# Performance work log

Measured on AMD Instinct MI355X. Metric: run time of the kernel, lower is better.

## Reference

```python
import jax, jax.numpy as jnp
import numpy as np

B, N, DIM = 4, 2048, 64  # batch, seq_len (== gate out dim), model dim (== dim_head)
H, DH = 8, 64            # heads, dim_head


def setup_inputs() -> dict:
    key = jax.random.key(0)
    ks = jax.random.split(key, 12)
    inner = H * DH
    inp = {
        'q': jax.random.normal(ks[0], (B, N, DIM), jnp.float32),
        'k': jax.random.normal(ks[1], (B, N, DIM), jnp.float32),
        'v': jax.random.normal(ks[2], (B, N, DIM), jnp.float32),
        'Wq': jax.random.normal(ks[3], (inner, DIM), jnp.float32) * 0.05,
        'Wk': jax.random.normal(ks[4], (inner, DIM), jnp.float32) * 0.05,
        'Wv': jax.random.normal(ks[5], (inner, DIM), jnp.float32) * 0.05,
        'Wo': jax.random.normal(ks[6], (DIM, inner), jnp.float32) * 0.05,
        'bo': jax.random.normal(ks[7], (DIM,), jnp.float32) * 0.05,
        'Wg': jax.random.normal(ks[8], (N, DIM), jnp.float32) * 0.05,
        's_local': jnp.float32(1.0),
        's_long': jnp.float32(1.0),
        # recurrent compressive-memory state; positive to avoid 0/0 of zero-init buffers
        'mem': jax.random.uniform(ks[9], (H, DH, DH), jnp.float32) + 0.5,
        'mem_norm': jax.random.uniform(ks[10], (H, N, 1), jnp.float32) + 0.5,
    }
    return inp


def _heads(x, W):
    # x: (B,N,DIM) @ W.T (DIM, H*DH) -> (B,H,N,DH)
    y = x @ W.T
    return y.reshape(x.shape[0], x.shape[1], H, DH).transpose(0, 2, 1, 3)


def reference(q, k, v, Wq, Wk, Wv, Wo, bo, Wg, s_local, s_long, mem, mem_norm):
    scale = DH ** -0.5
    qh, kh, vh = _heads(q, Wq), _heads(k, Wk), _heads(v, Wv)  # (B,H,N,DH)

    # local softmax attention, down-gated by (1 - sigmoid(local scalar))
    sim = jnp.einsum('bhnd,bhmd->bhnm', qh, kh) * scale
    local_attn = jax.nn.softmax(sim, axis=-1) * (1.0 - jax.nn.sigmoid(s_local))

    # query compressive memory: elu(q) @ M / (elu(q) * norm)
    eq = jax.nn.elu(qh)
    mem_q = jnp.einsum('bhnd,hde->bhne', eq, mem) / (eq * mem_norm[None])  # (B,H,N,DH)
    gated = jax.nn.sigmoid(s_long) * jnp.einsum('bhnd,md->bhnm', mem_q, Wg)  # (B,H,N,N)

    attn = local_attn + gated
    out = jnp.einsum('bhnm,bhmd->bhnd', attn, vh)
    out = out.transpose(0, 2, 1, 3).reshape(q.shape[0], q.shape[1], H * DH)
    out = out @ Wo.T + bo  # (B,N,DIM)

    # memory update (state side effect in the original forward)
    ek = jax.nn.elu(kh)
    v_term = vh - jnp.einsum('bhnd,hde->bhne', ek, mem) / (ek * mem_norm[None])
    new_mem = mem[None] + jnp.einsum('bhnd,bhne->bhde', ek, v_term)  # (B,H,DH,DH)
    new_norm = ek.sum(-1)  # (B,H,N)
    return out, new_mem, new_norm
```

## Files before the change

### kernel.cpp

```cpp
#include <hip/hip_runtime.h>
#include <math.h>


#define B_   4
#define N_   2048
#define H_   8
#define BH_  32
#define KP   72

typedef __bf16 bf16x8 __attribute__((ext_vector_type(8)));
typedef __bf16 bf16x4 __attribute__((ext_vector_type(4)));
typedef float  f32x4  __attribute__((ext_vector_type(4)));

__device__ __forceinline__ float eluf(float x) {
    return x > 0.0f ? x : expm1f(x);
}

__global__ __launch_bounds__(256) void k_proj(
    const float* __restrict__ q, const float* __restrict__ k, const float* __restrict__ v,
    const float* __restrict__ Wq, const float* __restrict__ Wk, const float* __restrict__ Wv,
    __bf16* __restrict__ qb, float* __restrict__ kh, __bf16* __restrict__ kb,
    __bf16* __restrict__ vb, __bf16* __restrict__ vbT)
{
    const int which = blockIdx.z;
    const float* __restrict__ src = (which == 0) ? q : (which == 1) ? k : v;
    const float* __restrict__ W   = (which == 0) ? Wq : (which == 1) ? Wk : Wv;
    const int h    = blockIdx.y;
    const int row0 = blockIdx.x * 64;

    __shared__ __align__(16) float AsT[64][68];
    __shared__ __align__(16) float WsT[64][68];
    const int tid = threadIdx.x;
    for (int s = 0; s < 16; ++s) {
        int flat = s * 256 + tid;
        int r = flat >> 6, d = flat & 63;
        AsT[d][r] = src[(size_t)(row0 + r) * 64 + d];
        WsT[d][r] = W[(size_t)(h * 64 + r) * 64 + d];
    }
    __syncthreads();

    const int ty = tid >> 4, tx = tid & 15;
    float acc[4][4];
    #pragma unroll
    for (int i = 0; i < 4; ++i)
        #pragma unroll
        for (int j = 0; j < 4; ++j) acc[i][j] = 0.0f;
    for (int kd = 0; kd < 64; ++kd) {
        float4 a4 = *(const float4*)&AsT[kd][ty * 4];
        float4 w4 = *(const float4*)&WsT[kd][tx * 4];
        float a[4] = {a4.x, a4.y, a4.z, a4.w};
        float w[4] = {w4.x, w4.y, w4.z, w4.w};
        #pragma unroll
        for (int i = 0; i < 4; ++i)
            #pragma unroll
            for (int j = 0; j < 4; ++j) acc[i][j] = fmaf(a[i], w[j], acc[i][j]);
    }

    const int b = row0 >> 11, nb = row0 & 2047;
    if (which == 0) {
        #pragma unroll
        for (int i = 0; i < 4; ++i) {
            size_t idx = ((((size_t)b * H_ + h) * N_ + nb + ty * 4 + i) << 6) + tx * 4;
            bf16x4 o4 = {(__bf16)acc[i][0], (__bf16)acc[i][1],
                         (__bf16)acc[i][2], (__bf16)acc[i][3]};
            *(bf16x4*)&qb[idx] = o4;
        }
    } else if (which == 1) {
        #pragma unroll
        for (int i = 0; i < 4; ++i) {
            size_t idx = ((((size_t)b * H_ + h) * N_ + nb + ty * 4 + i) << 6) + tx * 4;
            *(float4*)&kh[idx] = make_float4(acc[i][0], acc[i][1], acc[i][2], acc[i][3]);
            bf16x4 o4 = {(__bf16)acc[i][0], (__bf16)acc[i][1],
                         (__bf16)acc[i][2], (__bf16)acc[i][3]};
            *(bf16x4*)&kb[idx] = o4;
        }
    } else {
        #pragma unroll
        for (int i = 0; i < 4; ++i) {
            size_t idx = ((((size_t)b * H_ + h) * N_ + nb + ty * 4 + i) << 6) + tx * 4;
            bf16x4 o4 = {(__bf16)acc[i][0], (__bf16)acc[i][1],
                         (__bf16)acc[i][2], (__bf16)acc[i][3]};
            *(bf16x4*)&vb[idx] = o4;
        }
        __syncthreads();
        #pragma unroll
        for (int i = 0; i < 4; ++i)
            #pragma unroll
            for (int j = 0; j < 4; ++j) WsT[tx * 4 + j][ty * 4 + i] = acc[i][j];
        __syncthreads();
        const int e = tid >> 2, nc = (tid & 3) * 16;
        bf16x8 lo, hi;
        #pragma unroll
        for (int jj = 0; jj < 8; ++jj) {
            lo[jj] = (__bf16)WsT[e][nc + jj];
            hi[jj] = (__bf16)WsT[e][nc + 8 + jj];
        }
        size_t base = (((size_t)b * H_ + h) * 64 + e) * (size_t)N_ + nb + nc;
        *(bf16x8*)&vbT[base]     = lo;
        *(bf16x8*)&vbT[base + 8] = hi;
    }
}

__global__ __launch_bounds__(256) void k_memacc(
    const float* __restrict__ kh, const __bf16* __restrict__ vb,
    const float* __restrict__ mem, const float* __restrict__ mem_norm,
    float* __restrict__ pmem, float* __restrict__ out_norm)
{
    const int chunk = blockIdx.x;
    const int bh    = blockIdx.y;
    const int h     = bh & 7;
    const int n0    = chunk * 128;

    __shared__ __align__(16) __bf16 memT_hi[64 * KP], memT_lo[64 * KP];
    __shared__ __align__(16) __bf16 ekn_hi[64 * KP],  ekn_lo[64 * KP];
    __shared__ __align__(16) __bf16 ekT_hi[64 * KP],  ekT_lo[64 * KP];
    __shared__ __align__(16) __bf16 vtT_hi[64 * KP],  vtT_lo[64 * KP];

    const int tid  = threadIdx.x;
    const int w    = tid >> 6, lane = tid & 63;
    const int quad = lane >> 4, m = lane & 15;

    for (int s = 0; s < 16; ++s) {
        int flat = s * 256 + tid;
        int d = flat >> 6, e = flat & 63;
        float mv = mem[(size_t)h * 4096 + flat];
        __bf16 hi = (__bf16)mv;
        memT_hi[e * KP + d] = hi;
        memT_lo[e * KP + d] = (__bf16)(mv - (float)hi);
    }

    f32x4 accM[4];
    #pragma unroll
    for (int t = 0; t < 4; ++t) { f32x4 z = {0.f, 0.f, 0.f, 0.f}; accM[t] = z; }
    __syncthreads();

    for (int sub = 0; sub < 2; ++sub) {
        const int nb = n0 + sub * 64;
        for (int rr = w; rr < 64; rr += 4) {
            const int n = nb + rr;
            float ekv = eluf(kh[((size_t)bh * N_ + n) * 64 + lane]);
            __bf16 hi = (__bf16)ekv;
            __bf16 lo = (__bf16)(ekv - (float)hi);
            ekn_hi[rr * KP + lane] = hi;
            ekn_lo[rr * KP + lane] = lo;
            ekT_hi[lane * KP + rr] = hi;
            ekT_lo[lane * KP + rr] = lo;
            float srt = ekv;
            #pragma unroll
            for (int m2 = 32; m2; m2 >>= 1) srt += __shfl_xor(srt, m2, 64);
            if (lane == 0) out_norm[(size_t)bh * N_ + n] = srt;
        }
        __syncthreads();

        f32x4 km[4];
        #pragma unroll
        for (int t = 0; t < 4; ++t) { f32x4 z = {0.f, 0.f, 0.f, 0.f}; km[t] = z; }
        #pragma unroll
        for (int c2 = 0; c2 < 2; ++c2) {
            bf16x8 Ah = *(const bf16x8*)&ekn_hi[(w * 16 + m) * KP + c2 * 32 + quad * 8];
            bf16x8 Al = *(const bf16x8*)&ekn_lo[(w * 16 + m) * KP + c2 * 32 + quad * 8];
            #pragma unroll
            for (int et = 0; et < 4; ++et) {
                bf16x8 Bh = *(const bf16x8*)&memT_hi[(et * 16 + m) * KP + c2 * 32 + quad * 8];
                bf16x8 Bl = *(const bf16x8*)&memT_lo[(et * 16 + m) * KP + c2 * 32 + quad * 8];
                km[et] = __builtin_amdgcn_mfma_f32_16x16x32_bf16(Al, Bh, km[et], 0, 0, 0);
                km[et] = __builtin_amdgcn_mfma_f32_16x16x32_bf16(Ah, Bl, km[et], 0, 0, 0);
                km[et] = __builtin_amdgcn_mfma_f32_16x16x32_bf16(Ah, Bh, km[et], 0, 0, 0);
            }
        }
        float nrmv[4];
        #pragma unroll
        for (int r = 0; r < 4; ++r)
            nrmv[r] = mem_norm[(size_t)h * N_ + nb + w * 16 + quad * 4 + r];
        #pragma unroll
        for (int et = 0; et < 4; ++et) {
            #pragma unroll
            for (int r = 0; r < 4; ++r) {
                const int nl = w * 16 + quad * 4 + r;
                const int e  = et * 16 + m;
                float vh  = (float)vb[((size_t)bh * N_ + nb + nl) * 64 + e];
                float ekv = (float)ekn_hi[nl * KP + e] + (float)ekn_lo[nl * KP + e];
                float vt  = vh - km[et][r] / (ekv * nrmv[r]);
                __bf16 hi = (__bf16)vt;
                vtT_hi[e * KP + nl] = hi;
                vtT_lo[e * KP + nl] = (__bf16)(vt - (float)hi);
            }
        }
        __syncthreads();

        #pragma unroll
        for (int c2 = 0; c2 < 2; ++c2) {
            bf16x8 Ah = *(const bf16x8*)&ekT_hi[(w * 16 + m) * KP + c2 * 32 + quad * 8];
            bf16x8 Al = *(const bf16x8*)&ekT_lo[(w * 16 + m) * KP + c2 * 32 + quad * 8];
            #pragma unroll
            for (int et = 0; et < 4; ++et) {
                bf16x8 Bh = *(const bf16x8*)&vtT_hi[(et * 16 + m) * KP + c2 * 32 + quad * 8];
                bf16x8 Bl = *(const bf16x8*)&vtT_lo[(et * 16 + m) * KP + c2 * 32 + quad * 8];
                accM[et] = __builtin_amdgcn_mfma_f32_16x16x32_bf16(Al, Bh, accM[et], 0, 0, 0);
                accM[et] = __builtin_amdgcn_mfma_f32_16x16x32_bf16(Ah, Bl, accM[et], 0, 0, 0);
                accM[et] = __builtin_amdgcn_mfma_f32_16x16x32_bf16(Ah, Bh, accM[et], 0, 0, 0);
            }
        }
        __syncthreads();
    }

    const size_t base = ((size_t)chunk * BH_ + bh) * 4096;
    #pragma unroll
    for (int et = 0; et < 4; ++et)
        #pragma unroll
        for (int r = 0; r < 4; ++r)
            pmem[base + (size_t)(w * 16 + quad * 4 + r) * 64 + et * 16 + m] =
                accM[et][r];
}

__global__ __launch_bounds__(256) void k_gv(
    const float* __restrict__ Wg, const __bf16* __restrict__ vbT,
    float* __restrict__ pGv)
{
    const int chunk = blockIdx.x;
    const int bh    = blockIdx.y;
    const int n0    = chunk * 128;
    __shared__ __align__(16) __bf16 WgT[64 * 136];
    const int tid  = threadIdx.x;
    const int w    = tid >> 6, lane = tid & 63;
    const int quad = lane >> 4, m = tid & 15;

    for (int s = 0; s < 8; ++s) {
        int f4 = s * 256 + tid;
        int n = f4 >> 4, dg = (f4 & 15) * 4;
        float4 wv = *(const float4*)&Wg[(size_t)(n0 + n) * 64 + dg];
        WgT[(dg + 0) * 136 + n] = (__bf16)wv.x;
        WgT[(dg + 1) * 136 + n] = (__bf16)wv.y;
        WgT[(dg + 2) * 136 + n] = (__bf16)wv.z;
        WgT[(dg + 3) * 136 + n] = (__bf16)wv.w;
    }
    __syncthreads();

    f32x4 acc[4];
    #pragma unroll
    for (int t = 0; t < 4; ++t) { f32x4 z = {0.f, 0.f, 0.f, 0.f}; acc[t] = z; }
    #pragma unroll
    for (int c = 0; c < 4; ++c) {
        bf16x8 Af = *(const bf16x8*)&WgT[(w * 16 + m) * 136 + c * 32 + quad * 8];
        #pragma unroll
        for (int et = 0; et < 4; ++et) {
            bf16x8 Bf = *(const bf16x8*)&vbT[((size_t)bh * 64 + et * 16 + m) * N_ +
                                             n0 + c * 32 + quad * 8];
            acc[et] = __builtin_amdgcn_mfma_f32_16x16x32_bf16(Af, Bf, acc[et], 0, 0, 0);
        }
    }
    const size_t base = ((size_t)chunk * BH_ + bh) * 4096;
    #pragma unroll
    for (int et = 0; et < 4; ++et)
        #pragma unroll
        for (int r = 0; r < 4; ++r)
            pGv[base + (size_t)(w * 16 + quad * 4 + r) * 64 + et * 16 + m] =
                acc[et][r];
}

__global__ __launch_bounds__(256) void k_reduce(
    const float* __restrict__ mem, const float* __restrict__ pmem,
    const float* __restrict__ pGv, float* __restrict__ out_mem, float* __restrict__ Gv)
{
    const int idx = blockIdx.x * 256 + threadIdx.x;
    const int bh = idx >> 12, h = bh & 7, de = idx & 4095;
    float sm = mem[(size_t)h * 4096 + de];
    float sg = 0.0f;
    #pragma unroll
    for (int c = 0; c < 16; ++c) {
        sm += pmem[(size_t)c * 131072 + idx];
        sg += pGv[(size_t)c * 131072 + idx];
    }
    out_mem[idx] = sm;
    Gv[idx] = sg;
}

__global__ __launch_bounds__(256, 4) void k_flash(
    const __bf16* __restrict__ qb, const __bf16* __restrict__ kb,
    const __bf16* __restrict__ vbT, const float* __restrict__ mem,
    const float* __restrict__ mem_norm, const float* __restrict__ Gv,
    const float* __restrict__ s_local_p, const float* __restrict__ s_long_p,
    __bf16* __restrict__ o)
{
    const int n0 = blockIdx.x * 128;
    const int bh = blockIdx.y;
    const int h  = bh & 7;
    const __bf16* __restrict__ kbp = kb  + (size_t)bh * N_ * 64;
    const __bf16* __restrict__ vtp = vbT + (size_t)bh * 64 * N_;

    __shared__ __align__(16) __bf16 Kb[64 * KP];
    __shared__ __align__(16) __bf16 VT[64 * KP];
    __shared__ __align__(16) __bf16 Pw[128 * KP];
    __shared__ float lsl[128];
    __shared__ float nrm_l[128];

    const int tid  = threadIdx.x;
    const int w    = tid >> 6, lane = tid & 63;
    const int quad = lane >> 4, m = lane & 15;
    const float gl   = 1.0f - 1.0f / (1.0f + __expf(-s_local_p[0]));
    const float sigg = 1.0f / (1.0f + __expf(-s_long_p[0]));

    if (tid < 128) nrm_l[tid] = mem_norm[(size_t)h * N_ + n0 + tid];

    const size_t q0 = ((size_t)bh * N_ + n0 + w * 32 + m) * 64;
    const size_t q1 = q0 + 16 * 64;
    bf16x8 qa00 = *(const bf16x8*)&qb[q0 + quad * 8];
    bf16x8 qa01 = *(const bf16x8*)&qb[q0 + 32 + quad * 8];
    bf16x8 qa10 = *(const bf16x8*)&qb[q1 + quad * 8];
    bf16x8 qa11 = *(const bf16x8*)&qb[q1 + 32 + quad * 8];

    f32x4 O0[4], O1[4];
    #pragma unroll
    for (int t = 0; t < 4; ++t) {
        f32x4 z = {0.f, 0.f, 0.f, 0.f};
        O0[t] = z; O1[t] = z;
    }
    float lsum0 = 0.f, lsum1 = 0.f;
    const int pr0 = w * 32, pr1 = w * 32 + 16;

    const int srow = tid >> 2, scg = (tid & 3) * 16;
    bf16x8 pk0 = *(const bf16x8*)&kbp[(size_t)srow * 64 + scg];
    bf16x8 pk1 = *(const bf16x8*)&kbp[(size_t)srow * 64 + scg + 8];
    bf16x8 pv0 = *(const bf16x8*)&vtp[(size_t)srow * N_ + scg];
    bf16x8 pv1 = *(const bf16x8*)&vtp[(size_t)srow * N_ + scg + 8];

    for (int c = 0; c < 32; ++c) {
        __syncthreads();
        *(bf16x8*)&Kb[srow * KP + scg]     = pk0;
        *(bf16x8*)&Kb[srow * KP + scg + 8] = pk1;
        *(bf16x8*)&VT[srow * KP + scg]     = pv0;
        *(bf16x8*)&VT[srow * KP + scg + 8] = pv1;
        __syncthreads();
        if (c + 1 < 32) {
            const size_t kn = (size_t)((c + 1) * 64 + srow) * 64 + scg;
            const size_t vn = (size_t)srow * N_ + (c + 1) * 64 + scg;
            pk0 = *(const bf16x8*)&kbp[kn];
            pk1 = *(const bf16x8*)&kbp[kn + 8];
            pv0 = *(const bf16x8*)&vtp[vn];
            pv1 = *(const bf16x8*)&vtp[vn + 8];
        }

        f32x4 s0[4], s1[4];
        #pragma unroll
        for (int t = 0; t < 4; ++t) {
            bf16x8 ka0 = *(const bf16x8*)&Kb[(t * 16 + m) * KP + quad * 8];
            bf16x8 ka1 = *(const bf16x8*)&Kb[(t * 16 + m) * KP + 32 + quad * 8];
            f32x4 z = {0.f, 0.f, 0.f, 0.f};
            z = __builtin_amdgcn_mfma_f32_16x16x32_bf16(ka0, qa00, z, 0, 0, 0);
            s0[t] = __builtin_amdgcn_mfma_f32_16x16x32_bf16(ka1, qa01, z, 0, 0, 0);
            f32x4 z2 = {0.f, 0.f, 0.f, 0.f};
            z2 = __builtin_amdgcn_mfma_f32_16x16x32_bf16(ka0, qa10, z2, 0, 0, 0);
            s1[t] = __builtin_amdgcn_mfma_f32_16x16x32_bf16(ka1, qa11, z2, 0, 0, 0);
        }

        #pragma unroll
        for (int t = 0; t < 4; ++t) {
            float p0 = __expf(s0[t][0] * 0.125f), p1 = __expf(s0[t][1] * 0.125f);
            float p2 = __expf(s0[t][2] * 0.125f), p3 = __expf(s0[t][3] * 0.125f);
            lsum0 += p0 + p1 + p2 + p3;
            bf16x4 pk = {(__bf16)p0, (__bf16)p1, (__bf16)p2, (__bf16)p3};
            *(bf16x4*)&Pw[(pr0 + m) * KP + t * 16 + quad * 4] = pk;
            float r0 = __expf(s1[t][0] * 0.125f), r1 = __expf(s1[t][1] * 0.125f);
            float r2 = __expf(s1[t][2] * 0.125f), r3 = __expf(s1[t][3] * 0.125f);
            lsum1 += r0 + r1 + r2 + r3;
            bf16x4 rk = {(__bf16)r0, (__bf16)r1, (__bf16)r2, (__bf16)r3};
            *(bf16x4*)&Pw[(pr1 + m) * KP + t * 16 + quad * 4] = rk;
        }
        asm volatile("s_waitcnt lgkmcnt(0)" ::: "memory");

        #pragma unroll
        for (int c2 = 0; c2 < 2; ++c2) {
            bf16x8 pa0 = *(const bf16x8*)&Pw[(pr0 + m) * KP + c2 * 32 + quad * 8];
            bf16x8 pa1 = *(const bf16x8*)&Pw[(pr1 + m) * KP + c2 * 32 + quad * 8];
            #pragma unroll
            for (int t = 0; t < 4; ++t) {
                bf16x8 vv = *(const bf16x8*)&VT[(t * 16 + m) * KP + c2 * 32 + quad * 8];
                O0[t] = __builtin_amdgcn_mfma_f32_16x16x32_bf16(pa0, vv, O0[t], 0, 0, 0);
                O1[t] = __builtin_amdgcn_mfma_f32_16x16x32_bf16(pa1, vv, O1[t], 0, 0, 0);
            }
        }
    }

    lsum0 += __shfl_xor(lsum0, 16, 64); lsum0 += __shfl_xor(lsum0, 32, 64);
    lsum1 += __shfl_xor(lsum1, 16, 64); lsum1 += __shfl_xor(lsum1, 32, 64);
    if (lane < 16) { lsl[pr0 + lane] = lsum0; lsl[pr1 + lane] = lsum1; }

    __syncthreads();
    for (int s2 = 0; s2 < 16; ++s2) {
        int flat = s2 * 256 + tid;
        int d = flat >> 6, e = flat & 63;
        Kb[e * KP + d] = (__bf16)mem[(size_t)h * 4096 + flat];
        VT[e * KP + d] = (__bf16)Gv[(size_t)bh * 4096 + flat];
    }
    __syncthreads();

    __bf16* op = o + ((size_t)bh * N_ + n0) * 64;
    #pragma unroll
    for (int s = 0; s < 2; ++s) {
        const int prs = w * 32 + s * 16;
        bf16x8 ea0, ea1;
        #pragma unroll
        for (int j = 0; j < 8; ++j) {
            ea0[j] = (__bf16)eluf((float)(s == 0 ? qa00[j] : qa10[j]));
            ea1[j] = (__bf16)eluf((float)(s == 0 ? qa01[j] : qa11[j]));
        }
        f32x4 num[4];
        #pragma unroll
        for (int t = 0; t < 4; ++t) {
            bf16x8 b0 = *(const bf16x8*)&Kb[(t * 16 + m) * KP + quad * 8];
            bf16x8 b1 = *(const bf16x8*)&Kb[(t * 16 + m) * KP + 32 + quad * 8];
            f32x4 z = {0.f, 0.f, 0.f, 0.f};
            z = __builtin_amdgcn_mfma_f32_16x16x32_bf16(ea0, b0, z, 0, 0, 0);
            num[t] = __builtin_amdgcn_mfma_f32_16x16x32_bf16(ea1, b1, z, 0, 0, 0);
        }
        *(bf16x8*)&Pw[(prs + m) * KP + quad * 8]      = ea0;
        *(bf16x8*)&Pw[(prs + m) * KP + 32 + quad * 8] = ea1;
        asm volatile("s_waitcnt lgkmcnt(0)" ::: "memory");
        float mq[4][4];
        #pragma unroll
        for (int t = 0; t < 4; ++t)
            #pragma unroll
            for (int r = 0; r < 4; ++r) {
                float eqv = (float)Pw[(prs + quad * 4 + r) * KP + t * 16 + m];
                mq[t][r] = num[t][r] / (eqv * nrm_l[prs + quad * 4 + r]);
            }
        #pragma unroll
        for (int t = 0; t < 4; ++t)
            #pragma unroll
            for (int r = 0; r < 4; ++r)
                Pw[(prs + quad * 4 + r) * KP + t * 16 + m] = (__bf16)mq[t][r];
        asm volatile("s_waitcnt lgkmcnt(0)" ::: "memory");
        bf16x8 ma0 = *(const bf16x8*)&Pw[(prs + m) * KP + quad * 8];
        bf16x8 ma1 = *(const bf16x8*)&Pw[(prs + m) * KP + 32 + quad * 8];

        #pragma unroll
        for (int t = 0; t < 4; ++t) {
            bf16x8 g0 = *(const bf16x8*)&VT[(t * 16 + m) * KP + quad * 8];
            bf16x8 g1 = *(const bf16x8*)&VT[(t * 16 + m) * KP + 32 + quad * 8];
            f32x4 z = {0.f, 0.f, 0.f, 0.f};
            z = __builtin_amdgcn_mfma_f32_16x16x32_bf16(ma0, g0, z, 0, 0, 0);
            f32x4 o2 = __builtin_amdgcn_mfma_f32_16x16x32_bf16(ma1, g1, z, 0, 0, 0);
            const f32x4 Oc = (s == 0) ? O0[t] : O1[t];
            #pragma unroll
            for (int r = 0; r < 4; ++r) {
                const int qr = prs + quad * 4 + r;
                float val = Oc[r] * (gl / lsl[qr]) + sigg * o2[r];
                op[(size_t)qr * 64 + t * 16 + m] = (__bf16)val;
            }
        }
    }
}

__global__ __launch_bounds__(256) void k_outproj(
    const __bf16* __restrict__ o, const float* __restrict__ Wo,
    const float* __restrict__ bo, float* __restrict__ out)
{
    const int row0 = blockIdx.x * 64;
    const int b = row0 >> 11, nb = row0 & 2047;
    __shared__ __align__(16) __bf16 WoS[64 * 40];
    const int tid  = threadIdx.x;
    const int w    = tid >> 6, lane = tid & 63;
    const int quad = lane >> 4, m = lane & 15;

    f32x4 acc[4];
    #pragma unroll
    for (int t = 0; t < 4; ++t) { f32x4 z = {0.f, 0.f, 0.f, 0.f}; acc[t] = z; }

    for (int kbk = 0; kbk < 16; ++kbk) {
        for (int s2 = 0; s2 < 8; ++s2) {
            int flat = s2 * 256 + tid;
            int n = flat >> 5, kk = flat & 31;
            WoS[n * 40 + kk] = (__bf16)Wo[(size_t)n * 512 + kbk * 32 + kk];
        }
        __syncthreads();
        const int hc = kbk >> 1;
        size_t arow = (((size_t)b * H_ + hc) * N_ + nb + w * 16 + m);
        bf16x8 af = *(const bf16x8*)&o[arow * 64 + (kbk & 1) * 32 + quad * 8];
        #pragma unroll
        for (int t = 0; t < 4; ++t) {
            bf16x8 bf_ = *(const bf16x8*)&WoS[(t * 16 + m) * 40 + quad * 8];
            acc[t] = __builtin_amdgcn_mfma_f32_16x16x32_bf16(af, bf_, acc[t], 0, 0, 0);
        }
        __syncthreads();
    }
    #pragma unroll
    for (int t = 0; t < 4; ++t) {
        float bias = bo[t * 16 + m];
        #pragma unroll
        for (int r = 0; r < 4; ++r)
            out[(size_t)(row0 + w * 16 + quad * 4 + r) * 64 + t * 16 + m] =
                acc[t][r] + bias;
    }
}

extern "C" void kernel_launch(void* const* d_in, const int* in_sizes, int n_in,
                              void* d_out, int out_size, void* d_ws, size_t ws_size,
                              hipStream_t stream)
{
    const float* q        = (const float*)d_in[0];
    const float* k        = (const float*)d_in[1];
    const float* v        = (const float*)d_in[2];
    const float* Wq       = (const float*)d_in[3];
    const float* Wk       = (const float*)d_in[4];
    const float* Wv       = (const float*)d_in[5];
    const float* Wo       = (const float*)d_in[6];
    const float* bo       = (const float*)d_in[7];
    const float* Wg       = (const float*)d_in[8];
    const float* s_local  = (const float*)d_in[9];
    const float* s_long   = (const float*)d_in[10];
    const float* mem      = (const float*)d_in[11];
    const float* mem_norm = (const float*)d_in[12];

    float* ws = (float*)d_ws;
    float*  kh  = ws;
    __bf16* qb  = (__bf16*)(ws + 4194304);
    __bf16* kb  = (__bf16*)(ws + 6291456);
    __bf16* vb  = (__bf16*)(ws + 8388608);
    __bf16* vbT = (__bf16*)(ws + 10485760);
    float*  Gv  = ws + 12582912;
    float*  pm  = ws + 12713984;
    float*  pg  = ws + 14811136;
    __bf16* o   = (__bf16*)(ws + 12713984);

    float* out      = (float*)d_out;
    float* out_mem  = out + 524288;
    float* out_norm = out + 655360;

    k_proj   <<<dim3(128, 8, 3), 256, 0, stream>>>(q, k, v, Wq, Wk, Wv,
                                                   qb, kh, kb, vb, vbT);
    k_memacc <<<dim3(16, 32),    256, 0, stream>>>(kh, vb, mem, mem_norm,
                                                   pm, out_norm);
    k_gv     <<<dim3(16, 32),    256, 0, stream>>>(Wg, vbT, pg);
    k_reduce <<<dim3(512),       256, 0, stream>>>(mem, pm, pg, out_mem, Gv);
    k_flash  <<<dim3(16, 32),    256, 0, stream>>>(qb, kb, vbT, mem, mem_norm, Gv,
                                                   s_local, s_long, o);
    k_outproj<<<dim3(128),       256, 0, stream>>>(o, Wo, bo, out);
}
```

Measured before the change: 221.7 us.

## Double-buffer K/V tiles via global_load_lds with XOR-swizzled layout

```diff
diff --git a/kernel.cpp b/kernel.cpp
--- a/kernel.cpp
+++ b/kernel.cpp
@@ -14,6 +14,12 @@
 
 __device__ __forceinline__ float eluf(float x) {
     return x > 0.0f ? x : expm1f(x);
+}
+
+__device__ __forceinline__ void gl2lds16(const void* g, void* l) {
+    __builtin_amdgcn_global_load_lds(
+        (const __attribute__((address_space(1))) unsigned int*)g,
+        (__attribute__((address_space(3))) unsigned int*)l, 16, 0, 0);
 }
 
 __global__ __launch_bounds__(256) void k_proj(
@@ -68,11 +74,13 @@
     } else if (which == 1) {
         #pragma unroll
         for (int i = 0; i < 4; ++i) {
-            size_t idx = ((((size_t)b * H_ + h) * N_ + nb + ty * 4 + i) << 6) + tx * 4;
-            *(float4*)&kh[idx] = make_float4(acc[i][0], acc[i][1], acc[i][2], acc[i][3]);
+            size_t rowbase = (((size_t)b * H_ + h) * N_ + nb + ty * 4 + i) << 6;
+            *(float4*)&kh[rowbase + tx * 4] =
+                make_float4(acc[i][0], acc[i][1], acc[i][2], acc[i][3]);
             bf16x4 o4 = {(__bf16)acc[i][0], (__bf16)acc[i][1],
                          (__bf16)acc[i][2], (__bf16)acc[i][3]};
-            *(bf16x4*)&kb[idx] = o4;
+            const int s = (ty * 4 + i) & 7;
+            *(bf16x4*)&kb[rowbase + (((tx >> 1) ^ s) << 3) + (tx & 1) * 4] = o4;
         }
     } else {
         #pragma unroll
@@ -95,9 +103,11 @@
             lo[jj] = (__bf16)WsT[e][nc + jj];
             hi[jj] = (__bf16)WsT[e][nc + 8 + jj];
         }
-        size_t base = (((size_t)b * H_ + h) * 64 + e) * (size_t)N_ + nb + nc;
-        *(bf16x8*)&vbT[base]     = lo;
-        *(bf16x8*)&vbT[base + 8] = hi;
+        size_t rowb = (((size_t)b * H_ + h) * 64 + e) * (size_t)N_ + nb;
+        const int j0 = (nc >> 3) ^ (e & 7);
+        const int j1 = ((nc >> 3) + 1) ^ (e & 7);
+        *(bf16x8*)&vbT[rowb + j0 * 8] = lo;
+        *(bf16x8*)&vbT[rowb + j1 * 8] = hi;
     }
 }
 
@@ -244,8 +254,9 @@
         bf16x8 Af = *(const bf16x8*)&WgT[(w * 16 + m) * 136 + c * 32 + quad * 8];
         #pragma unroll
         for (int et = 0; et < 4; ++et) {
+            const int jb = ((4 * c + quad) & 7) ^ (m & 7);
             bf16x8 Bf = *(const bf16x8*)&vbT[((size_t)bh * 64 + et * 16 + m) * N_ +
-                                             n0 + c * 32 + quad * 8];
+                                             n0 + (c >> 1) * 64 + jb * 8];
             acc[et] = __builtin_amdgcn_mfma_f32_16x16x32_bf16(Af, Bf, acc[et], 0, 0, 0);
         }
     }
@@ -288,8 +299,8 @@
     const __bf16* __restrict__ kbp = kb  + (size_t)bh * N_ * 64;
     const __bf16* __restrict__ vtp = vbT + (size_t)bh * 64 * N_;
 
-    __shared__ __align__(16) __bf16 Kb[64 * KP];
-    __shared__ __align__(16) __bf16 VT[64 * KP];
+    __shared__ __align__(16) __bf16 Kt[2][64 * 64];
+    __shared__ __align__(16) __bf16 Vt[2][64 * 64];
     __shared__ __align__(16) __bf16 Pw[128 * KP];
     __shared__ float lsl[128];
     __shared__ float nrm_l[128];
@@ -297,8 +308,10 @@
     const int tid  = threadIdx.x;
     const int w    = tid >> 6, lane = tid & 63;
     const int quad = lane >> 4, m = lane & 15;
+    const int sw   = m & 7;
     const float gl   = 1.0f - 1.0f / (1.0f + __expf(-s_local_p[0]));
     const float sigg = 1.0f / (1.0f + __expf(-s_long_p[0]));
+    const float SCL  = 0.18033688f;
 
     if (tid < 128) nrm_l[tid] = mem_norm[(size_t)h * N_ + n0 + tid];
 
@@ -318,33 +331,38 @@
     float lsum0 = 0.f, lsum1 = 0.f;
     const int pr0 = w * 32, pr1 = w * 32 + 16;
 
-    const int srow = tid >> 2, scg = (tid & 3) * 16;
-    bf16x8 pk0 = *(const bf16x8*)&kbp[(size_t)srow * 64 + scg];
-    bf16x8 pk1 = *(const bf16x8*)&kbp[(size_t)srow * 64 + scg + 8];
-    bf16x8 pv0 = *(const bf16x8*)&vtp[(size_t)srow * N_ + scg];
-    bf16x8 pv1 = *(const bf16x8*)&vtp[(size_t)srow * N_ + scg + 8];
+    const int r0 = w * 16 + (lane >> 3);
+    auto stage = [&](int c, int buf) {
+        const __bf16* gk0 = kbp + ((size_t)c * 64 + r0) * 64 + (lane & 7) * 8;
+        const __bf16* gv0 = vtp + (size_t)r0 * N_ + c * 64 + (lane & 7) * 8;
+        char* lk = (char*)&Kt[buf][0] + w * 2048;
+        char* lv = (char*)&Vt[buf][0] + w * 2048;
+        gl2lds16(gk0,            lk);
+        gl2lds16(gk0 + 8 * 64,   lk + 1024);
+        gl2lds16(gv0,            lv);
+        gl2lds16(gv0 + 8 * N_,   lv + 1024);
+    };
+
+    stage(0, 0);
 
     for (int c = 0; c < 32; ++c) {
-        __syncthreads();
-        *(bf16x8*)&Kb[srow * KP + scg]     = pk0;
-        *(bf16x8*)&Kb[srow * KP + scg + 8] = pk1;
-        *(bf16x8*)&VT[srow * KP + scg]     = pv0;
-        *(bf16x8*)&VT[srow * KP + scg + 8] = pv1;
-        __syncthreads();
+        const int buf = c & 1;
+        asm volatile("s_barrier" ::: "memory");
         if (c + 1 < 32) {
-            const size_t kn = (size_t)((c + 1) * 64 + srow) * 64 + scg;
-            const size_t vn = (size_t)srow * N_ + (c + 1) * 64 + scg;
-            pk0 = *(const bf16x8*)&kbp[kn];
-            pk1 = *(const bf16x8*)&kbp[kn + 8];
-            pv0 = *(const bf16x8*)&vtp[vn];
-            pv1 = *(const bf16x8*)&vtp[vn + 8];
-        }
+            stage(c + 1, buf ^ 1);
+            asm volatile("s_waitcnt vmcnt(4)" ::: "memory");
+        } else {
+            asm volatile("s_waitcnt vmcnt(0)" ::: "memory");
+        }
+        asm volatile("s_barrier" ::: "memory");
+        const __bf16* Kc = &Kt[buf][0];
+        const __bf16* Vc = &Vt[buf][0];
 
         f32x4 s0[4], s1[4];
         #pragma unroll
         for (int t = 0; t < 4; ++t) {
-            bf16x8 ka0 = *(const bf16x8*)&Kb[(t * 16 + m) * KP + quad * 8];
-            bf16x8 ka1 = *(const bf16x8*)&Kb[(t * 16 + m) * KP + 32 + quad * 8];
+            bf16x8 ka0 = *(const bf16x8*)&Kc[(t * 16 + m) * 64 + ((quad ^ sw) << 3)];
+            bf16x8 ka1 = *(const bf16x8*)&Kc[(t * 16 + m) * 64 + (((4 + quad) ^ sw) << 3)];
             f32x4 z = {0.f, 0.f, 0.f, 0.f};
             z = __builtin_amdgcn_mfma_f32_16x16x32_bf16(ka0, qa00, z, 0, 0, 0);
             s0[t] = __builtin_amdgcn_mfma_f32_16x16x32_bf16(ka1, qa01, z, 0, 0, 0);
@@ -355,15 +373,15 @@
 
         #pragma unroll
         for (int t = 0; t < 4; ++t) {
-            float p0 = __expf(s0[t][0] * 0.125f), p1 = __expf(s0[t][1] * 0.125f);
-            float p2 = __expf(s0[t][2] * 0.125f), p3 = __expf(s0[t][3] * 0.125f);
+            float p0 = exp2f(s0[t][0] * SCL), p1 = exp2f(s0[t][1] * SCL);
+            float p2 = exp2f(s0[t][2] * SCL), p3 = exp2f(s0[t][3] * SCL);
             lsum0 += p0 + p1 + p2 + p3;
             bf16x4 pk = {(__bf16)p0, (__bf16)p1, (__bf16)p2, (__bf16)p3};
             *(bf16x4*)&Pw[(pr0 + m) * KP + t * 16 + quad * 4] = pk;
-            float r0 = __expf(s1[t][0] * 0.125f), r1 = __expf(s1[t][1] * 0.125f);
-            float r2 = __expf(s1[t][2] * 0.125f), r3 = __expf(s1[t][3] * 0.125f);
-            lsum1 += r0 + r1 + r2 + r3;
-            bf16x4 rk = {(__bf16)r0, (__bf16)r1, (__bf16)r2, (__bf16)r3};
+            float r0_ = exp2f(s1[t][0] * SCL), r1_ = exp2f(s1[t][1] * SCL);
+            float r2_ = exp2f(s1[t][2] * SCL), r3_ = exp2f(s1[t][3] * SCL);
+            lsum1 += r0_ + r1_ + r2_ + r3_;
+            bf16x4 rk = {(__bf16)r0_, (__bf16)r1_, (__bf16)r2_, (__bf16)r3_};
             *(bf16x4*)&Pw[(pr1 + m) * KP + t * 16 + quad * 4] = rk;
         }
         asm volatile("s_waitcnt lgkmcnt(0)" ::: "memory");
@@ -374,7 +392,8 @@
             bf16x8 pa1 = *(const bf16x8*)&Pw[(pr1 + m) * KP + c2 * 32 + quad * 8];
             #pragma unroll
             for (int t = 0; t < 4; ++t) {
-                bf16x8 vv = *(const bf16x8*)&VT[(t * 16 + m) * KP + c2 * 32 + quad * 8];
+                bf16x8 vv = *(const bf16x8*)&Vc[(t * 16 + m) * 64 +
+                                                (((c2 * 4 + quad) ^ sw) << 3)];
                 O0[t] = __builtin_amdgcn_mfma_f32_16x16x32_bf16(pa0, vv, O0[t], 0, 0, 0);
                 O1[t] = __builtin_amdgcn_mfma_f32_16x16x32_bf16(pa1, vv, O1[t], 0, 0, 0);
             }
@@ -386,11 +405,13 @@
     if (lane < 16) { lsl[pr0 + lane] = lsum0; lsl[pr1 + lane] = lsum1; }
 
     __syncthreads();
+    __bf16* MT = &Kt[0][0];
+    __bf16* GT = &Vt[0][0];
     for (int s2 = 0; s2 < 16; ++s2) {
         int flat = s2 * 256 + tid;
         int d = flat >> 6, e = flat & 63;
-        Kb[e * KP + d] = (__bf16)mem[(size_t)h * 4096 + flat];
-        VT[e * KP + d] = (__bf16)Gv[(size_t)bh * 4096 + flat];
+        MT[e * KP + d] = (__bf16)mem[(size_t)h * 4096 + flat];
+        GT[e * KP + d] = (__bf16)Gv[(size_t)bh * 4096 + flat];
     }
     __syncthreads();
 
@@ -407,8 +428,8 @@
         f32x4 num[4];
         #pragma unroll
         for (int t = 0; t < 4; ++t) {
-            bf16x8 b0 = *(const bf16x8*)&Kb[(t * 16 + m) * KP + quad * 8];
-            bf16x8 b1 = *(const bf16x8*)&Kb[(t * 16 + m) * KP + 32 + quad * 8];
+            bf16x8 b0 = *(const bf16x8*)&MT[(t * 16 + m) * KP + quad * 8];
+            bf16x8 b1 = *(const bf16x8*)&MT[(t * 16 + m) * KP + 32 + quad * 8];
             f32x4 z = {0.f, 0.f, 0.f, 0.f};
             z = __builtin_amdgcn_mfma_f32_16x16x32_bf16(ea0, b0, z, 0, 0, 0);
             num[t] = __builtin_amdgcn_mfma_f32_16x16x32_bf16(ea1, b1, z, 0, 0, 0);
@@ -435,16 +456,16 @@
 
         #pragma unroll
         for (int t = 0; t < 4; ++t) {
-            bf16x8 g0 = *(const bf16x8*)&VT[(t * 16 + m) * KP + quad * 8];
-            bf16x8 g1 = *(const bf16x8*)&VT[(t * 16 + m) * KP + 32 + quad * 8];
+            bf16x8 g0 = *(const bf16x8*)&GT[(t * 16 + m) * KP + quad * 8];
+            bf16x8 g1 = *(const bf16x8*)&GT[(t * 16 + m) * KP + 32 + quad * 8];
             f32x4 z = {0.f, 0.f, 0.f, 0.f};
             z = __builtin_amdgcn_mfma_f32_16x16x32_bf16(ma0, g0, z, 0, 0, 0);
             f32x4 o2 = __builtin_amdgcn_mfma_f32_16x16x32_bf16(ma1, g1, z, 0, 0, 0);
-            const f32x4 Oc = (s == 0) ? O0[t] : O1[t];
             #pragma unroll
             for (int r = 0; r < 4; ++r) {
                 const int qr = prs + quad * 4 + r;
-                float val = Oc[r] * (gl / lsl[qr]) + sigg * o2[r];
+                float val = ((s == 0) ? O0[t][r] : O1[t][r]) * (gl / lsl[qr])
+                            + sigg * o2[r];
                 op[(size_t)qr * 64 + t * 16 + m] = (__bf16)val;
             }
         }
```

After: 237.1 us. 6.9% more time.

## Split flash attention over key halves and add separate combine kernel

Applied to the files above, without the earlier changes.

```diff
diff --git a/kernel.cpp b/kernel.cpp
--- a/kernel.cpp
+++ b/kernel.cpp
@@ -277,30 +277,23 @@
 
 __global__ __launch_bounds__(256, 4) void k_flash(
     const __bf16* __restrict__ qb, const __bf16* __restrict__ kb,
-    const __bf16* __restrict__ vbT, const float* __restrict__ mem,
-    const float* __restrict__ mem_norm, const float* __restrict__ Gv,
-    const float* __restrict__ s_local_p, const float* __restrict__ s_long_p,
-    __bf16* __restrict__ o)
-{
-    const int n0 = blockIdx.x * 128;
-    const int bh = blockIdx.y;
-    const int h  = bh & 7;
+    const __bf16* __restrict__ vbT, __bf16* __restrict__ Opart,
+    float* __restrict__ lsp)
+{
+    const int n0   = blockIdx.x * 128;
+    const int half = blockIdx.y;
+    const int bh   = blockIdx.z;
     const __bf16* __restrict__ kbp = kb  + (size_t)bh * N_ * 64;
     const __bf16* __restrict__ vtp = vbT + (size_t)bh * 64 * N_;
 
     __shared__ __align__(16) __bf16 Kb[64 * KP];
     __shared__ __align__(16) __bf16 VT[64 * KP];
     __shared__ __align__(16) __bf16 Pw[128 * KP];
-    __shared__ float lsl[128];
-    __shared__ float nrm_l[128];
 
     const int tid  = threadIdx.x;
     const int w    = tid >> 6, lane = tid & 63;
     const int quad = lane >> 4, m = lane & 15;
-    const float gl   = 1.0f - 1.0f / (1.0f + __expf(-s_local_p[0]));
-    const float sigg = 1.0f / (1.0f + __expf(-s_long_p[0]));
-
-    if (tid < 128) nrm_l[tid] = mem_norm[(size_t)h * N_ + n0 + tid];
+    const float SCL = 0.18033688f;
 
     const size_t q0 = ((size_t)bh * N_ + n0 + w * 32 + m) * 64;
     const size_t q1 = q0 + 16 * 64;
@@ -319,19 +312,21 @@
     const int pr0 = w * 32, pr1 = w * 32 + 16;
 
     const int srow = tid >> 2, scg = (tid & 3) * 16;
-    bf16x8 pk0 = *(const bf16x8*)&kbp[(size_t)srow * 64 + scg];
-    bf16x8 pk1 = *(const bf16x8*)&kbp[(size_t)srow * 64 + scg + 8];
-    bf16x8 pv0 = *(const bf16x8*)&vtp[(size_t)srow * N_ + scg];
-    bf16x8 pv1 = *(const bf16x8*)&vtp[(size_t)srow * N_ + scg + 8];
-
-    for (int c = 0; c < 32; ++c) {
+    const int c0 = half * 16;
+    bf16x8 pk0 = *(const bf16x8*)&kbp[(size_t)(c0 * 64 + srow) * 64 + scg];
+    bf16x8 pk1 = *(const bf16x8*)&kbp[(size_t)(c0 * 64 + srow) * 64 + scg + 8];
+    bf16x8 pv0 = *(const bf16x8*)&vtp[(size_t)srow * N_ + c0 * 64 + scg];
+    bf16x8 pv1 = *(const bf16x8*)&vtp[(size_t)srow * N_ + c0 * 64 + scg + 8];
+
+    for (int cc = 0; cc < 16; ++cc) {
+        const int c = c0 + cc;
         __syncthreads();
         *(bf16x8*)&Kb[srow * KP + scg]     = pk0;
         *(bf16x8*)&Kb[srow * KP + scg + 8] = pk1;
         *(bf16x8*)&VT[srow * KP + scg]     = pv0;
         *(bf16x8*)&VT[srow * KP + scg + 8] = pv1;
         __syncthreads();
-        if (c + 1 < 32) {
+        if (cc + 1 < 16) {
             const size_t kn = (size_t)((c + 1) * 64 + srow) * 64 + scg;
             const size_t vn = (size_t)srow * N_ + (c + 1) * 64 + scg;
             pk0 = *(const bf16x8*)&kbp[kn];
@@ -355,13 +350,13 @@
 
         #pragma unroll
         for (int t = 0; t < 4; ++t) {
-            float p0 = __expf(s0[t][0] * 0.125f), p1 = __expf(s0[t][1] * 0.125f);
-            float p2 = __expf(s0[t][2] * 0.125f), p3 = __expf(s0[t][3] * 0.125f);
+            float p0 = exp2f(s0[t][0] * SCL), p1 = exp2f(s0[t][1] * SCL);
+            float p2 = exp2f(s0[t][2] * SCL), p3 = exp2f(s0[t][3] * SCL);
             lsum0 += p0 + p1 + p2 + p3;
             bf16x4 pk = {(__bf16)p0, (__bf16)p1, (__bf16)p2, (__bf16)p3};
             *(bf16x4*)&Pw[(pr0 + m) * KP + t * 16 + quad * 4] = pk;
-            float r0 = __expf(s1[t][0] * 0.125f), r1 = __expf(s1[t][1] * 0.125f);
-            float r2 = __expf(s1[t][2] * 0.125f), r3 = __expf(s1[t][3] * 0.125f);
+            float r0 = exp2f(s1[t][0] * SCL), r1 = exp2f(s1[t][1] * SCL);
+            float r2 = exp2f(s1[t][2] * SCL), r3 = exp2f(s1[t][3] * SCL);
             lsum1 += r0 + r1 + r2 + r3;
             bf16x4 rk = {(__bf16)r0, (__bf16)r1, (__bf16)r2, (__bf16)r3};
             *(bf16x4*)&Pw[(pr1 + m) * KP + t * 16 + quad * 4] = rk;
@@ -383,72 +378,133 @@
 
     lsum0 += __shfl_xor(lsum0, 16, 64); lsum0 += __shfl_xor(lsum0, 32, 64);
     lsum1 += __shfl_xor(lsum1, 16, 64); lsum1 += __shfl_xor(lsum1, 32, 64);
-    if (lane < 16) { lsl[pr0 + lane] = lsum0; lsl[pr1 + lane] = lsum1; }
-
-    __syncthreads();
+    const size_t lbase = ((size_t)half * BH_ + bh) * N_ + n0;
+    if (lane < 16) {
+        lsp[lbase + pr0 + lane] = lsum0;
+        lsp[lbase + pr1 + lane] = lsum1;
+    }
+
+    __bf16* op = Opart + (((size_t)half * BH_ + bh) * N_ + n0) * 64;
+    #pragma unroll
+    for (int t = 0; t < 4; ++t)
+        #pragma unroll
+        for (int r = 0; r < 4; ++r) {
+            op[(size_t)(pr0 + quad * 4 + r) * 64 + t * 16 + m] = (__bf16)O0[t][r];
+            op[(size_t)(pr1 + quad * 4 + r) * 64 + t * 16 + m] = (__bf16)O1[t][r];
+        }
+}
+
+__global__ __launch_bounds__(256, 4) void k_combine(
+    const __bf16* __restrict__ Opart, const float* __restrict__ lsp,
+    const __bf16* __restrict__ qb, const float* __restrict__ mem,
+    const float* __restrict__ mem_norm, const float* __restrict__ Gv,
+    const float* __restrict__ s_local_p, const float* __restrict__ s_long_p,
+    __bf16* __restrict__ o)
+{
+    const int n0 = blockIdx.x * 64;
+    const int bh = blockIdx.y;
+    const int h  = bh & 7;
+
+    __shared__ __align__(16) __bf16 MT[64 * KP];
+    __shared__ __align__(16) __bf16 GT[64 * KP];
+    __shared__ __align__(16) __bf16 Pc[64 * KP];
+    __shared__ float lsl[64];
+    __shared__ float nrm_l[64];
+
+    const int tid  = threadIdx.x;
+    const int w    = tid >> 6, lane = tid & 63;
+    const int quad = lane >> 4, m = lane & 15;
+    const float gl   = 1.0f - 1.0f / (1.0f + __expf(-s_local_p[0]));
+    const float sigg = 1.0f / (1.0f + __expf(-s_long_p[0]));
+
+    if (tid < 64) {
+        lsl[tid] = lsp[(size_t)bh * N_ + n0 + tid] +
+                   lsp[((size_t)BH_ + bh) * N_ + n0 + tid];
+        nrm_l[tid] = mem_norm[(size_t)h * N_ + n0 + tid];
+    }
     for (int s2 = 0; s2 < 16; ++s2) {
         int flat = s2 * 256 + tid;
         int d = flat >> 6, e = flat & 63;
-        Kb[e * KP + d] = (__bf16)mem[(size_t)h * 4096 + flat];
-        VT[e * KP + d] = (__bf16)Gv[(size_t)bh * 4096 + flat];
+        MT[e * KP + d] = (__bf16)mem[(size_t)h * 4096 + flat];
+        GT[e * KP + d] = (__bf16)Gv[(size_t)bh * 4096 + flat];
     }
     __syncthreads();
 
-    __bf16* op = o + ((size_t)bh * N_ + n0) * 64;
-    #pragma unroll
-    for (int s = 0; s < 2; ++s) {
-        const int prs = w * 32 + s * 16;
-        bf16x8 ea0, ea1;
-        #pragma unroll
-        for (int j = 0; j < 8; ++j) {
-            ea0[j] = (__bf16)eluf((float)(s == 0 ? qa00[j] : qa10[j]));
-            ea1[j] = (__bf16)eluf((float)(s == 0 ? qa01[j] : qa11[j]));
-        }
-        f32x4 num[4];
-        #pragma unroll
-        for (int t = 0; t < 4; ++t) {
-            bf16x8 b0 = *(const bf16x8*)&Kb[(t * 16 + m) * KP + quad * 8];
-            bf16x8 b1 = *(const bf16x8*)&Kb[(t * 16 + m) * KP + 32 + quad * 8];
-            f32x4 z = {0.f, 0.f, 0.f, 0.f};
-            z = __builtin_amdgcn_mfma_f32_16x16x32_bf16(ea0, b0, z, 0, 0, 0);
-            num[t] = __builtin_amdgcn_mfma_f32_16x16x32_bf16(ea1, b1, z, 0, 0, 0);
-        }
-        *(bf16x8*)&Pw[(prs + m) * KP + quad * 8]      = ea0;
-        *(bf16x8*)&Pw[(prs + m) * KP + 32 + quad * 8] = ea1;
-        asm volatile("s_waitcnt lgkmcnt(0)" ::: "memory");
-        float mq[4][4];
-        #pragma unroll
-        for (int t = 0; t < 4; ++t)
-            #pragma unroll
-            for (int r = 0; r < 4; ++r) {
-                float eqv = (float)Pw[(prs + quad * 4 + r) * KP + t * 16 + m];
-                mq[t][r] = num[t][r] / (eqv * nrm_l[prs + quad * 4 + r]);
-            }
-        #pragma unroll
-        for (int t = 0; t < 4; ++t)
-            #pragma unroll
-            for (int r = 0; r < 4; ++r)
-                Pw[(prs + quad * 4 + r) * KP + t * 16 + m] = (__bf16)mq[t][r];
-        asm volatile("s_waitcnt lgkmcnt(0)" ::: "memory");
-        bf16x8 ma0 = *(const bf16x8*)&Pw[(prs + m) * KP + quad * 8];
-        bf16x8 ma1 = *(const bf16x8*)&Pw[(prs + m) * KP + 32 + quad * 8];
-
-        #pragma unroll
-        for (int t = 0; t < 4; ++t) {
-            bf16x8 g0 = *(const bf16x8*)&VT[(t * 16 + m) * KP + quad * 8];
-            bf16x8 g1 = *(const bf16x8*)&VT[(t * 16 + m) * KP + 32 + quad * 8];
-            f32x4 z = {0.f, 0.f, 0.f, 0.f};
-            z = __builtin_amdgcn_mfma_f32_16x16x32_bf16(ma0, g0, z, 0, 0, 0);
-            f32x4 o2 = __builtin_amdgcn_mfma_f32_16x16x32_bf16(ma1, g1, z, 0, 0, 0);
-            const f32x4 Oc = (s == 0) ? O0[t] : O1[t];
-            #pragma unroll
-            for (int r = 0; r < 4; ++r) {
-                const int qr = prs + quad * 4 + r;
-                float val = Oc[r] * (gl / lsl[qr]) + sigg * o2[r];
-                op[(size_t)qr * 64 + t * 16 + m] = (__bf16)val;
-            }
-        }
-    }
+    const int prow = w * 16;
+    const size_t qo = ((size_t)bh * N_ + n0 + prow + m) * 64;
+    bf16x8 qa0 = *(const bf16x8*)&qb[qo + quad * 8];
+    bf16x8 qa1 = *(const bf16x8*)&qb[qo + 32 + quad * 8];
+    bf16x8 ea0, ea1;
+    #pragma unroll
+    for (int j = 0; j < 8; ++j) {
+        ea0[j] = (__bf16)eluf((float)qa0[j]);
+        ea1[j] = (__bf16)eluf((float)qa1[j]);
+    }
+    f32x4 num[4];
+    #pragma unroll
+    for (int t = 0; t < 4; ++t) {
+        bf16x8 b0 = *(const bf16x8*)&MT[(t * 16 + m) * KP + quad * 8];
+        bf16x8 b1 = *(const bf16x8*)&MT[(t * 16 + m) * KP + 32 + quad * 8];
+        f32x4 z = {0.f, 0.f, 0.f, 0.f};
+        z = __builtin_amdgcn_mfma_f32_16x16x32_bf16(ea0, b0, z, 0, 0, 0);
+        num[t] = __builtin_amdgcn_mfma_f32_16x16x32_bf16(ea1, b1, z, 0, 0, 0);
+    }
+    *(bf16x8*)&Pc[(prow + m) * KP + quad * 8]      = ea0;
+    *(bf16x8*)&Pc[(prow + m) * KP + 32 + quad * 8] = ea1;
+    asm volatile("s_waitcnt lgkmcnt(0)" ::: "memory");
+    float mq[4][4];
+    #pragma unroll
+    for (int t = 0; t < 4; ++t)
+        #pragma unroll
+        for (int r = 0; r < 4; ++r) {
+            float eqv = (float)Pc[(prow + quad * 4 + r) * KP + t * 16 + m];
+            mq[t][r] = num[t][r] / (eqv * nrm_l[prow + quad * 4 + r]);
+        }
+    #pragma unroll
+    for (int t = 0; t < 4; ++t)
+        #pragma unroll
+        for (int r = 0; r < 4; ++r)
+            Pc[(prow + quad * 4 + r) * KP + t * 16 + m] = (__bf16)mq[t][r];
+    asm volatile("s_waitcnt lgkmcnt(0)" ::: "memory");
+    bf16x8 ma0 = *(const bf16x8*)&Pc[(prow + m) * KP + quad * 8];
+    bf16x8 ma1 = *(const bf16x8*)&Pc[(prow + m) * KP + 32 + quad * 8];
+    __syncthreads();
+
+    f32x4 o2[4];
+    #pragma unroll
+    for (int t = 0; t < 4; ++t) {
+        bf16x8 g0 = *(const bf16x8*)&GT[(t * 16 + m) * KP + quad * 8];
+        bf16x8 g1 = *(const bf16x8*)&GT[(t * 16 + m) * KP + 32 + quad * 8];
+        f32x4 z = {0.f, 0.f, 0.f, 0.f};
+        z = __builtin_amdgcn_mfma_f32_16x16x32_bf16(ma0, g0, z, 0, 0, 0);
+        o2[t] = __builtin_amdgcn_mfma_f32_16x16x32_bf16(ma1, g1, z, 0, 0, 0);
+    }
+    #pragma unroll
+    for (int t = 0; t < 4; ++t) {
+        bf16x4 pk = {(__bf16)(sigg * o2[t][0]), (__bf16)(sigg * o2[t][1]),
+                     (__bf16)(sigg * o2[t][2]), (__bf16)(sigg * o2[t][3])};
+        *(bf16x4*)&Pc[(t * 16 + m) * KP + prow + quad * 4] = pk;
+    }
+    __syncthreads();
+
+    const int row = tid >> 2, ec = (tid & 3) * 16;
+    const float scale = gl / lsl[row];
+    const size_t gbase = ((size_t)bh * N_ + n0 + row) * 64 + ec;
+    const size_t hoff  = (size_t)BH_ * N_ * 64;
+    bf16x8 a0 = *(const bf16x8*)&Opart[gbase];
+    bf16x8 a1 = *(const bf16x8*)&Opart[gbase + 8];
+    bf16x8 b0 = *(const bf16x8*)&Opart[hoff + gbase];
+    bf16x8 b1 = *(const bf16x8*)&Opart[hoff + gbase + 8];
+    bf16x8 r0, r1;
+    #pragma unroll
+    for (int j = 0; j < 8; ++j) {
+        r0[j] = (__bf16)(((float)a0[j] + (float)b0[j]) * scale +
+                         (float)Pc[(ec + j) * KP + row]);
+        r1[j] = (__bf16)(((float)a1[j] + (float)b1[j]) * scale +
+                         (float)Pc[(ec + 8 + j) * KP + row]);
+    }
+    *(bf16x8*)&o[gbase]     = r0;
+    *(bf16x8*)&o[gbase + 8] = r1;
 }
 
 __global__ __launch_bounds__(256) void k_outproj(
@@ -512,15 +568,17 @@
     const float* mem_norm = (const float*)d_in[12];
 
     float* ws = (float*)d_ws;
-    float*  kh  = ws;
-    __bf16* qb  = (__bf16*)(ws + 4194304);
-    __bf16* kb  = (__bf16*)(ws + 6291456);
-    __bf16* vb  = (__bf16*)(ws + 8388608);
-    __bf16* vbT = (__bf16*)(ws + 10485760);
-    float*  Gv  = ws + 12582912;
-    float*  pm  = ws + 12713984;
-    float*  pg  = ws + 14811136;
-    __bf16* o   = (__bf16*)(ws + 12713984);
+    float*  kh    = ws;
+    __bf16* Opart = (__bf16*)ws;
+    __bf16* qb    = (__bf16*)(ws + 4194304);
+    __bf16* kb    = (__bf16*)(ws + 6291456);
+    __bf16* vb    = (__bf16*)(ws + 8388608);
+    __bf16* vbT   = (__bf16*)(ws + 10485760);
+    float*  Gv    = ws + 12582912;
+    float*  pm    = ws + 12713984;
+    float*  pg    = ws + 14811136;
+    float*  lsp   = ws + 14811136;
+    __bf16* o     = (__bf16*)(ws + 12713984);
 
     float* out      = (float*)d_out;
     float* out_mem  = out + 524288;
@@ -532,7 +590,8 @@
                                                    pm, out_norm);
     k_gv     <<<dim3(16, 32),    256, 0, stream>>>(Wg, vbT, pg);
     k_reduce <<<dim3(512),       256, 0, stream>>>(mem, pm, pg, out_mem, Gv);
-    k_flash  <<<dim3(16, 32),    256, 0, stream>>>(qb, kb, vbT, mem, mem_norm, Gv,
-                                                   s_local, s_long, o);
+    k_flash  <<<dim3(16, 2, 32), 256, 0, stream>>>(qb, kb, vbT, Opart, lsp);
+    k_combine<<<dim3(32, 32),    256, 0, stream>>>(Opart, lsp, qb, mem, mem_norm,
+                                                   Gv, s_local, s_long, o);
     k_outproj<<<dim3(128),       256, 0, stream>>>(o, Wo, bo, out);
 }
```

Result: slower. 234.1 us (+5.6%).
